# Performance work log

Measured on AMD Instinct MI355X. Metric: run time of the kernel, lower is better.

Reference implementation:

```python
import jax, jax.numpy as jnp
import numpy as np

B, D, C = 8192, 256, 128
MARGIN = 0.5
REPULSION_WEIGHT = 1.0
ALPHA = 0.5
BETA = 0.5
EPS = 1e-6  # F.pairwise_distance default eps, added to the difference vector


def make_centers(num_classes=C, embedding_dim=D):
    # center[k] is +/-1 one-hot along axis (k % embedding_dim)
    idx = np.arange(num_classes)
    centers = np.zeros((num_classes, embedding_dim), dtype=np.float32)
    centers[idx, idx % embedding_dim] = np.where(idx % 2 == 0, 1.0, -1.0)
    return jnp.asarray(centers)


def setup_inputs() -> dict:
    key = jax.random.key(0)
    k1, k2, k3 = jax.random.split(key, 3)
    features = jax.random.normal(k1, (B, D), dtype=jnp.float32)
    classification = jax.random.normal(k2, (B, C), dtype=jnp.float32)
    labels = jax.random.randint(k3, (B,), 0, C, dtype=jnp.int32)
    return {"features": features, "classification": classification, "labels": labels}


def _sculpted_loss(embeddings, labels, centers):
    b = embeddings.shape[0]
    # attractive: MSE to per-sample class center, mean over all elements
    center_targets = centers[labels]  # [B, D]
    attractive = jnp.mean((embeddings - center_targets) ** 2)

    # repulsive: for pairs i<j with different labels,
    # relu(margin - ||e_i - e_j + eps||_2)^2, summed then / (B(B-1)/2).
    sq_norm = jnp.sum(embeddings ** 2, axis=1)          # [B]
    row_sum = jnp.sum(embeddings, axis=1)               # [B]
    gram = embeddings @ embeddings.T                    # [B, B]
    sq = (sq_norm[:, None] + sq_norm[None, :] - 2.0 * gram
          + 2.0 * EPS * (row_sum[:, None] - row_sum[None, :])
          + embeddings.shape[1] * (EPS * EPS))
    dist = jnp.sqrt(jnp.maximum(sq, 1e-12))             # [B, B]

    iu = jnp.triu(jnp.ones((b, b), dtype=bool), k=1)    # i < j
    diff_label = labels[:, None] != labels[None, :]
    mask = iu & diff_label
    hinge = jnp.maximum(MARGIN - dist, 0.0)
    repulsive = jnp.sum(jnp.where(mask, hinge * hinge, 0.0))
    repulsive = repulsive / (b * (b - 1) / 2.0)

    return attractive + REPULSION_WEIGHT * repulsive


def reference(features, classification, labels):
    centers = make_centers()
    # cross entropy (mean over batch)
    logp = jax.nn.log_softmax(classification, axis=-1)
    ce = -jnp.mean(jnp.take_along_axis(logp, labels[:, None].astype(jnp.int32), axis=1)[:, 0])
    contrastive = _sculpted_loss(features, labels, centers)
    return BETA * contrastive + ALPHA * ce
```

## Files before the change

kernel.cpp:

```cpp
#include <hip/hip_runtime.h>
#include <stdint.h>

#define B_N   8192
#define D_DIM 256
#define C_CLS 128
#define EPSV  1e-6f
#define DEPS  (256.0f * EPSV * EPSV)
#define NT    64
#define NTRI  (NT * (NT + 1) / 2)

typedef float f32x4 __attribute__((ext_vector_type(4)));

__device__ __forceinline__ unsigned f2fp8(float v) {
    unsigned u = __float_as_uint(v);
    unsigned s = (u >> 24) & 0x80;
    unsigned a = u & 0x7fffffff;
    if (a > 0x43E00000u) a = 0x43E00000u;
    a += 0x7FFFF + ((a >> 20) & 1);
    int e = (int)(a >> 23) - 120;
    if (e <= 0) return s;
    return s | ((unsigned)e << 3) | ((a >> 20) & 7);
}


__global__ __launch_bounds__(256) void k_prep(
        const float* __restrict__ feat, const float* __restrict__ cls,
        const int* __restrict__ labels, unsigned char* __restrict__ e8,
        float* __restrict__ aR, float* __restrict__ bC,
        float* __restrict__ attrP, float* __restrict__ ceP) {
    int t = threadIdx.x, lane = t & 63, w = t >> 6;
    int row = blockIdx.x * 4 + w;
    int lab = labels[row];

    const float4* src = (const float4*)(feat + (size_t)row * D_DIM);
    float4 f = src[lane];
    unsigned pk = f2fp8(f.x) | (f2fp8(f.y) << 8) | (f2fp8(f.z) << 16) | (f2fp8(f.w) << 24);
    ((unsigned*)(e8 + (size_t)row * D_DIM))[lane] = pk;

    float sq = f.x*f.x + f.y*f.y + f.z*f.z + f.w*f.w;
    float sm = f.x + f.y + f.z + f.w;
    float arr[4] = {f.x, f.y, f.z, f.w};
    float pick = ((lab >> 2) == lane) ? arr[lab & 3] : 0.f;

    const float2* csrc = (const float2*)(cls + (size_t)row * C_CLS);
    float2 c2 = csrc[lane];
    float mx = fmaxf(c2.x, c2.y);
    #pragma unroll
    for (int off = 32; off; off >>= 1) mx = fmaxf(mx, __shfl_xor(mx, off));
    float es = expf(c2.x - mx) + expf(c2.y - mx);
    float cpick = ((lab >> 1) == lane) ? ((lab & 1) ? c2.y : c2.x) : 0.f;

    #pragma unroll
    for (int off = 32; off; off >>= 1) {
        sq    += __shfl_xor(sq, off);
        sm    += __shfl_xor(sm, off);
        pick  += __shfl_xor(pick, off);
        es    += __shfl_xor(es, off);
        cpick += __shfl_xor(cpick, off);
    }
    __shared__ float wsumA[4], wsumC[4];
    if (lane == 0) {
        aR[row] = sq + 2.f * EPSV * sm;
        bC[row] = sq - 2.f * EPSV * sm + DEPS;
        float s = (lab & 1) ? -1.f : 1.f;
        wsumA[w] = sq - 2.f * s * pick + 1.f;
        wsumC[w] = -(cpick - mx - logf(es));
    }
    __syncthreads();
    if (t == 0) {
        attrP[blockIdx.x] = wsumA[0] + wsumA[1] + wsumA[2] + wsumA[3];
        ceP[blockIdx.x]   = wsumC[0] + wsumC[1] + wsumC[2] + wsumC[3];
    }
}

__global__ __launch_bounds__(256, 2) void k_gram(
        const unsigned char* __restrict__ e8, const float* __restrict__ aR,
        const float* __restrict__ bC, const int* __restrict__ labels,
        float* __restrict__ repP) {
    __shared__ __align__(16) unsigned char As[128 * 256];
    __shared__ __align__(16) unsigned char Bs[128 * 256];
    __shared__ float aM[128], bN[128];
    __shared__ int   lM[128], lN[128];
    __shared__ float wred[4];

    int t = threadIdx.x, lane = t & 63, w = t >> 6;

    int bid = blockIdx.x, tm = 0;
    while (bid >= NT - tm) { bid -= NT - tm; tm++; }
    int tn = tm + bid;

    if (t < 128) {
        int i = tm * 128 + t;
        aM[t] = aR[i]; lM[t] = labels[i];
    } else {
        int j = tn * 128 + (t - 128);
        bN[t - 128] = bC[j]; lN[t - 128] = labels[j];
    }

    int srow = t >> 4;
    int ulog = (lane & 15) ^ (srow & 15);
    #pragma unroll
    for (int i = 0; i < 8; i++) {
        int row = i * 16 + srow;
        const unsigned char* ga = e8 + (size_t)(tm * 128 + row) * D_DIM + ulog * 16;
        const unsigned char* gb = e8 + (size_t)(tn * 128 + row) * D_DIM + ulog * 16;
        unsigned char* la = As + i * 4096 + w * 1024;
        unsigned char* lb = Bs + i * 4096 + w * 1024;
        __builtin_amdgcn_global_load_lds((const __attribute__((address_space(1))) void*)ga,
                                         (__attribute__((address_space(3))) void*)la, 16, 0, 0);
        __builtin_amdgcn_global_load_lds((const __attribute__((address_space(1))) void*)gb,
                                         (__attribute__((address_space(3))) void*)lb, 16, 0, 0);
    }
    __syncthreads();

    f32x4 acc[4][4] = {};
    int wr = w >> 1, wc = w & 1;
    int quad = lane >> 4, l15 = lane & 15;
    int m0 = wr * 64, n0 = wc * 64;
    int half = (quad & 1) * 8, upair = quad >> 1;

    #pragma unroll
    for (int s = 0; s < 8; s++) {
        int ul = s * 2 + upair;
        long long av[4], bv[4];
        #pragma unroll
        for (int mi = 0; mi < 4; mi++) {
            int m = m0 + mi * 16 + l15;
            av[mi] = *(const long long*)(As + m * 256 + ((ul ^ l15) * 16) + half);
        }
        #pragma unroll
        for (int ni = 0; ni < 4; ni++) {
            int n = n0 + ni * 16 + l15;
            bv[ni] = *(const long long*)(Bs + n * 256 + ((ul ^ l15) * 16) + half);
        }
        #pragma unroll
        for (int mi = 0; mi < 4; mi++)
            #pragma unroll
            for (int ni = 0; ni < 4; ni++)
                acc[mi][ni] = __builtin_amdgcn_mfma_f32_16x16x32_fp8_fp8(av[mi], bv[ni], acc[mi][ni], 0, 0, 0);
    }

    float am[16], bn[4];
    #pragma unroll
    for (int ni = 0; ni < 4; ni++) bn[ni] = bN[wc * 64 + ni * 16 + l15];
    #pragma unroll
    for (int mi = 0; mi < 4; mi++)
        #pragma unroll
        for (int r = 0; r < 4; r++)
            am[mi * 4 + r] = aM[wr * 64 + mi * 16 + quad * 4 + r];

    float minv = 1e30f;
    #pragma unroll
    for (int mi = 0; mi < 4; mi++)
        #pragma unroll
        for (int ni = 0; ni < 4; ni++)
            #pragma unroll
            for (int r = 0; r < 4; r++)
                minv = fminf(minv, fmaf(-2.f, acc[mi][ni][r], am[mi * 4 + r] + bn[ni]));
    #pragma unroll
    for (int off = 32; off; off >>= 1) minv = fminf(minv, __shfl_xor(minv, off));

    float rep = 0.f;
    if (minv < 0.25f) {
        #pragma unroll
        for (int mi = 0; mi < 4; mi++) {
            #pragma unroll
            for (int ni = 0; ni < 4; ni++) {
                int n  = wc * 64 + ni * 16 + l15;
                int jg = tn * 128 + n;
                #pragma unroll
                for (int r = 0; r < 4; r++) {
                    int m  = wr * 64 + mi * 16 + quad * 4 + r;
                    int ig = tm * 128 + m;
                    float sq   = fmaf(-2.f, acc[mi][ni][r], am[mi * 4 + r] + bn[ni]);
                    float dist = sqrtf(fmaxf(sq, 1e-12f));
                    float h    = fmaxf(0.5f - dist, 0.f);
                    rep += (lM[m] != lN[n] && ig < jg) ? h * h : 0.f;
                }
            }
        }
        #pragma unroll
        for (int off = 32; off; off >>= 1) rep += __shfl_xor(rep, off);
    }
    if (lane == 0) wred[w] = rep;
    __syncthreads();
    if (t == 0) repP[blockIdx.x] = wred[0] + wred[1] + wred[2] + wred[3];
}

__global__ __launch_bounds__(256) void k_final(
        const float* __restrict__ P, float* __restrict__ out) {
    int t = threadIdx.x, lane = t & 63, w = t >> 6;
    float a = 0.f, c = 0.f, r = 0.f;
    for (int i = t; i < 2048; i += 256) { a += P[i]; c += P[2048 + i]; }
    for (int i = t; i < NTRI; i += 256) r += P[4096 + i];
    #pragma unroll
    for (int off = 32; off; off >>= 1) {
        a += __shfl_xor(a, off);
        c += __shfl_xor(c, off);
        r += __shfl_xor(r, off);
    }
    __shared__ float sa[4], sc[4], sr[4];
    if (lane == 0) { sa[w] = a; sc[w] = c; sr[w] = r; }
    __syncthreads();
    if (t == 0) {
        float attr = (sa[0] + sa[1] + sa[2] + sa[3]) / (float)((size_t)B_N * D_DIM);
        float ce   = (sc[0] + sc[1] + sc[2] + sc[3]) / (float)B_N;
        float rep  = (sr[0] + sr[1] + sr[2] + sr[3]) / ((float)B_N * (float)(B_N - 1) * 0.5f);
        out[0] = 0.5f * (attr + rep) + 0.5f * ce;
    }
}

extern "C" void kernel_launch(void* const* d_in, const int* in_sizes, int n_in,
                              void* d_out, int out_size, void* d_ws, size_t ws_size,
                              hipStream_t stream) {
    const float* feat   = (const float*)d_in[0];
    const float* cls    = (const float*)d_in[1];
    const int*   labels = (const int*)d_in[2];
    float* out = (float*)d_out;

    float*          P    = (float*)d_ws;
    unsigned char*  e8   = (unsigned char*)d_ws + 32768;
    float*          aR   = (float*)((char*)d_ws + 32768 + (size_t)B_N * D_DIM);
    float*          bC   = aR + B_N;
    float*          attrP = P;
    float*          ceP   = P + 2048;
    float*          repP  = P + 4096;

    k_prep <<<2048, 256, 0, stream>>>(feat, cls, labels, e8, aR, bC, attrP, ceP);
    k_gram <<<NTRI, 256, 0, stream>>>(e8, aR, bC, labels, repP);
    k_final<<<1, 256, 0, stream>>>(P, out);
}
```

Measured before the change: 99.26 us.

## Make gram kernel persistent with double-buffered LDS prefetch of next tile

Replaces the one-block-per-tile launch of 2080 blocks with 256 persistent blocks. Each block walks a contiguous run of 8-9 upper-triangular tiles and double-buffers the A and B fp8 tiles in 128KB of dynamic LDS, prefetching the next tile while the current one runs its MFMAs. The A tile is reloaded only when the tile row changes, and the per-row norms and labels are now read from global memory instead of being staged in LDS. This is meant to hide global-load latency and cut launch and tail overhead, at the cost of one block per CU occupancy and a serial dependence across tiles.

```diff
diff --git a/kernel.cpp b/kernel.cpp
--- a/kernel.cpp
+++ b/kernel.cpp
@@ -8,6 +8,8 @@
 #define DEPS  (256.0f * EPSV * EPSV)
 #define NT    64
 #define NTRI  (NT * (NT + 1) / 2)
+#define GBLK  256
+#define SMEM_BYTES (131072 + 64)
 
 typedef float f32x4 __attribute__((ext_vector_type(4)));
 
@@ -73,118 +75,148 @@
     }
 }
 
-__global__ __launch_bounds__(256, 2) void k_gram(
+__global__ __launch_bounds__(256) void k_gram(
         const unsigned char* __restrict__ e8, const float* __restrict__ aR,
         const float* __restrict__ bC, const int* __restrict__ labels,
         float* __restrict__ repP) {
-    __shared__ __align__(16) unsigned char As[128 * 256];
-    __shared__ __align__(16) unsigned char Bs[128 * 256];
-    __shared__ float aM[128], bN[128];
-    __shared__ int   lM[128], lN[128];
-    __shared__ float wred[4];
+    extern __shared__ __align__(16) unsigned char smem[];
 
     int t = threadIdx.x, lane = t & 63, w = t >> 6;
-
-    int bid = blockIdx.x, tm = 0;
-    while (bid >= NT - tm) { bid -= NT - tm; tm++; }
-    int tn = tm + bid;
-
-    if (t < 128) {
-        int i = tm * 128 + t;
-        aM[t] = aR[i]; lM[t] = labels[i];
-    } else {
-        int j = tn * 128 + (t - 128);
-        bN[t - 128] = bC[j]; lN[t - 128] = labels[j];
-    }
-
-    int srow = t >> 4;
-    int ulog = (lane & 15) ^ (srow & 15);
+    int b = blockIdx.x;
+    int start = b * 8 + (b < 32 ? b : 32);
+    int cnt   = 8 + (b < 32 ? 1 : 0);
+
+    int tm = 0, rem = start;
+    while (rem >= NT - tm) { rem -= NT - tm; tm++; }
+    int tn = tm + rem;
+
+    int srow  = t >> 4;
+    int sunit = t & 15;
+    int quad = lane >> 4, l15 = lane & 15;
+    int wr = w >> 1, wc = w & 1;
+    int m0 = wr * 64, n0 = wc * 64;
+    int half = (quad & 1) * 8, upair = quad >> 1;
+
     #pragma unroll
     for (int i = 0; i < 8; i++) {
         int row = i * 16 + srow;
-        const unsigned char* ga = e8 + (size_t)(tm * 128 + row) * D_DIM + ulog * 16;
-        const unsigned char* gb = e8 + (size_t)(tn * 128 + row) * D_DIM + ulog * 16;
-        unsigned char* la = As + i * 4096 + w * 1024;
-        unsigned char* lb = Bs + i * 4096 + w * 1024;
+        int uofs = ((sunit ^ (row & 15)) * 16);
+        const unsigned char* ga = e8 + (size_t)(tm * 128 + row) * D_DIM + uofs;
+        const unsigned char* gb = e8 + (size_t)(tn * 128 + row) * D_DIM + uofs;
         __builtin_amdgcn_global_load_lds((const __attribute__((address_space(1))) void*)ga,
-                                         (__attribute__((address_space(3))) void*)la, 16, 0, 0);
+            (__attribute__((address_space(3))) void*)(smem + i * 4096 + w * 1024), 16, 0, 0);
         __builtin_amdgcn_global_load_lds((const __attribute__((address_space(1))) void*)gb,
-                                         (__attribute__((address_space(3))) void*)lb, 16, 0, 0);
-    }
-    __syncthreads();
-
-    f32x4 acc[4][4] = {};
-    int wr = w >> 1, wc = w & 1;
-    int quad = lane >> 4, l15 = lane & 15;
-    int m0 = wr * 64, n0 = wc * 64;
-    int half = (quad & 1) * 8, upair = quad >> 1;
-
-    #pragma unroll
-    for (int s = 0; s < 8; s++) {
-        int ul = s * 2 + upair;
-        long long av[4], bv[4];
-        #pragma unroll
-        for (int mi = 0; mi < 4; mi++) {
-            int m = m0 + mi * 16 + l15;
-            av[mi] = *(const long long*)(As + m * 256 + ((ul ^ l15) * 16) + half);
-        }
-        #pragma unroll
-        for (int ni = 0; ni < 4; ni++) {
-            int n = n0 + ni * 16 + l15;
-            bv[ni] = *(const long long*)(Bs + n * 256 + ((ul ^ l15) * 16) + half);
-        }
-        #pragma unroll
-        for (int mi = 0; mi < 4; mi++)
-            #pragma unroll
-            for (int ni = 0; ni < 4; ni++)
-                acc[mi][ni] = __builtin_amdgcn_mfma_f32_16x16x32_fp8_fp8(av[mi], bv[ni], acc[mi][ni], 0, 0, 0);
-    }
-
-    float am[16], bn[4];
-    #pragma unroll
-    for (int ni = 0; ni < 4; ni++) bn[ni] = bN[wc * 64 + ni * 16 + l15];
-    #pragma unroll
-    for (int mi = 0; mi < 4; mi++)
-        #pragma unroll
-        for (int r = 0; r < 4; r++)
-            am[mi * 4 + r] = aM[wr * 64 + mi * 16 + quad * 4 + r];
-
-    float minv = 1e30f;
-    #pragma unroll
-    for (int mi = 0; mi < 4; mi++)
-        #pragma unroll
-        for (int ni = 0; ni < 4; ni++)
-            #pragma unroll
-            for (int r = 0; r < 4; r++)
-                minv = fminf(minv, fmaf(-2.f, acc[mi][ni][r], am[mi * 4 + r] + bn[ni]));
-    #pragma unroll
-    for (int off = 32; off; off >>= 1) minv = fminf(minv, __shfl_xor(minv, off));
-
+            (__attribute__((address_space(3))) void*)(smem + 65536 + i * 4096 + w * 1024), 16, 0, 0);
+    }
+    int cura = 0, curb = 0;
     float rep = 0.f;
-    if (minv < 0.25f) {
-        #pragma unroll
-        for (int mi = 0; mi < 4; mi++) {
-            #pragma unroll
-            for (int ni = 0; ni < 4; ni++) {
-                int n  = wc * 64 + ni * 16 + l15;
-                int jg = tn * 128 + n;
-                #pragma unroll
-                for (int r = 0; r < 4; r++) {
-                    int m  = wr * 64 + mi * 16 + quad * 4 + r;
-                    int ig = tm * 128 + m;
-                    float sq   = fmaf(-2.f, acc[mi][ni][r], am[mi * 4 + r] + bn[ni]);
-                    float dist = sqrtf(fmaxf(sq, 1e-12f));
-                    float h    = fmaxf(0.5f - dist, 0.f);
-                    rep += (lM[m] != lN[n] && ig < jg) ? h * h : 0.f;
+
+    for (int it = 0; it < cnt; it++) {
+        __syncthreads();
+
+        int ntm = tm, ntn = tn + 1;
+        if (ntn == NT) { ntm = tm + 1; ntn = ntm; }
+        bool havenext = (it + 1 < cnt);
+        if (havenext) {
+            if (ntm != tm) {
+                unsigned aoff = (cura ^ 1) * 32768u;
+                #pragma unroll
+                for (int i = 0; i < 8; i++) {
+                    int row = i * 16 + srow;
+                    const unsigned char* ga = e8 + (size_t)(ntm * 128 + row) * D_DIM
+                                              + ((sunit ^ (row & 15)) * 16);
+                    __builtin_amdgcn_global_load_lds((const __attribute__((address_space(1))) void*)ga,
+                        (__attribute__((address_space(3))) void*)(smem + aoff + i * 4096 + w * 1024), 16, 0, 0);
                 }
             }
-        }
-        #pragma unroll
-        for (int off = 32; off; off >>= 1) rep += __shfl_xor(rep, off);
-    }
+            unsigned boff = 65536u + (curb ^ 1) * 32768u;
+            #pragma unroll
+            for (int i = 0; i < 8; i++) {
+                int row = i * 16 + srow;
+                const unsigned char* gb = e8 + (size_t)(ntn * 128 + row) * D_DIM
+                                          + ((sunit ^ (row & 15)) * 16);
+                __builtin_amdgcn_global_load_lds((const __attribute__((address_space(1))) void*)gb,
+                    (__attribute__((address_space(3))) void*)(smem + boff + i * 4096 + w * 1024), 16, 0, 0);
+            }
+        }
+
+        const unsigned char* As = smem + cura * 32768u;
+        const unsigned char* Bs = smem + 65536u + curb * 32768u;
+        f32x4 acc[4][4] = {};
+        #pragma unroll
+        for (int s = 0; s < 8; s++) {
+            int ul = s * 2 + upair;
+            long long av[4], bv[4];
+            #pragma unroll
+            for (int mi = 0; mi < 4; mi++)
+                av[mi] = *(const long long*)(As + (m0 + mi * 16 + l15) * 256 + ((ul ^ l15) * 16) + half);
+            #pragma unroll
+            for (int ni = 0; ni < 4; ni++)
+                bv[ni] = *(const long long*)(Bs + (n0 + ni * 16 + l15) * 256 + ((ul ^ l15) * 16) + half);
+            #pragma unroll
+            for (int mi = 0; mi < 4; mi++)
+                #pragma unroll
+                for (int ni = 0; ni < 4; ni++)
+                    acc[mi][ni] = __builtin_amdgcn_mfma_f32_16x16x32_fp8_fp8(av[mi], bv[ni], acc[mi][ni], 0, 0, 0);
+        }
+
+        float bn[4]; int ln[4];
+        #pragma unroll
+        for (int ni = 0; ni < 4; ni++) {
+            int jg = tn * 128 + n0 + ni * 16 + l15;
+            bn[ni] = bC[jg]; ln[ni] = labels[jg];
+        }
+        float am[16]; int lm[16];
+        #pragma unroll
+        for (int mi = 0; mi < 4; mi++)
+            #pragma unroll
+            for (int r = 0; r < 4; r++) {
+                int ig = tm * 128 + m0 + mi * 16 + quad * 4 + r;
+                am[mi * 4 + r] = aR[ig]; lm[mi * 4 + r] = labels[ig];
+            }
+
+        float minv = 1e30f;
+        #pragma unroll
+        for (int mi = 0; mi < 4; mi++)
+            #pragma unroll
+            for (int ni = 0; ni < 4; ni++)
+                #pragma unroll
+                for (int r = 0; r < 4; r++)
+                    minv = fminf(minv, fmaf(-2.f, acc[mi][ni][r], am[mi * 4 + r] + bn[ni]));
+        #pragma unroll
+        for (int off = 32; off; off >>= 1) minv = fminf(minv, __shfl_xor(minv, off));
+
+        if (minv < 0.25f) {
+            #pragma unroll
+            for (int mi = 0; mi < 4; mi++)
+                #pragma unroll
+                for (int ni = 0; ni < 4; ni++) {
+                    int n  = n0 + ni * 16 + l15;
+                    int jg = tn * 128 + n;
+                    #pragma unroll
+                    for (int r = 0; r < 4; r++) {
+                        int ig = tm * 128 + m0 + mi * 16 + quad * 4 + r;
+                        float sq   = fmaf(-2.f, acc[mi][ni][r], am[mi * 4 + r] + bn[ni]);
+                        float dist = sqrtf(fmaxf(sq, 1e-12f));
+                        float h    = fmaxf(0.5f - dist, 0.f);
+                        rep += (lm[mi * 4 + r] != ln[ni] && ig < jg) ? h * h : 0.f;
+                    }
+                }
+        }
+
+        if (havenext) {
+            if (ntm != tm) cura ^= 1;
+            curb ^= 1;
+            tm = ntm; tn = ntn;
+        }
+    }
+
+    #pragma unroll
+    for (int off = 32; off; off >>= 1) rep += __shfl_xor(rep, off);
+    float* wred = (float*)(smem + 131072);
     if (lane == 0) wred[w] = rep;
     __syncthreads();
-    if (t == 0) repP[blockIdx.x] = wred[0] + wred[1] + wred[2] + wred[3];
+    if (t == 0) repP[b] = wred[0] + wred[1] + wred[2] + wred[3];
 }
 
 __global__ __launch_bounds__(256) void k_final(
@@ -192,7 +224,7 @@
     int t = threadIdx.x, lane = t & 63, w = t >> 6;
     float a = 0.f, c = 0.f, r = 0.f;
     for (int i = t; i < 2048; i += 256) { a += P[i]; c += P[2048 + i]; }
-    for (int i = t; i < NTRI; i += 256) r += P[4096 + i];
+    if (t < GBLK) r = P[4096 + t];
     #pragma unroll
     for (int off = 32; off; off >>= 1) {
         a += __shfl_xor(a, off);
@@ -226,7 +258,10 @@
     float*          ceP   = P + 2048;
     float*          repP  = P + 4096;
 
+    (void)hipFuncSetAttribute((const void*)k_gram,
+                              hipFuncAttributeMaxDynamicSharedMemorySize, SMEM_BYTES);
+
     k_prep <<<2048, 256, 0, stream>>>(feat, cls, labels, e8, aR, bC, attrP, ceP);
-    k_gram <<<NTRI, 256, 0, stream>>>(e8, aR, bC, labels, repP);
+    k_gram <<<GBLK, 256, SMEM_BYTES, stream>>>(e8, aR, bC, labels, repP);
     k_final<<<1, 256, 0, stream>>>(P, out);
 }
```

Result: slower. 108.4 us (+9.2%).
